# Optimization experiments

Measured on AMD Instinct MI355X. Metric: run time of the kernel, lower is better.

Reference implementation:

```python
import jax, jax.numpy as jnp
import numpy as np

K_SIZE = 5


def extract_patches(x, k):
    """tf.image.extract_patches(SAME, stride 1) -> [B, H, W, k*k, C].

    Kernel offsets are ordered row-major (ki, kj), matching TF's depth
    ordering (ki, kj, c) after the reshape in the original module.
    """
    pad = k // 2
    B, H, W, C = x.shape
    xp = jnp.pad(x, ((0, 0), (pad, pad), (pad, pad), (0, 0)))
    slices = [xp[:, i:i + H, j:j + W, :] for i in range(k) for j in range(k)]
    return jnp.stack(slices, axis=3)  # [B, H, W, k*k, C]


def setup_inputs() -> dict:
    key = jax.random.key(0)
    k1, k2, k3, k4, k5 = jax.random.split(key, 5)
    B, H, C, BIN = 4, 128, 128, 64
    return {
        "main": jax.random.normal(k1, (B, H, H, C), dtype=jnp.float32),
        "ref": jax.random.normal(k2, (B, H, H, C), dtype=jnp.float32),
        "ref_value": jax.random.normal(k3, (B, H, H, BIN), dtype=jnp.float32),
        "W_main": jax.random.normal(k4, (C, C), dtype=jnp.float32) * (2.0 / C) ** 0.5,
        "W_ref": jax.random.normal(k5, (C, C), dtype=jnp.float32) * (2.0 / C) ** 0.5,
    }


def reference(main, ref, ref_value, W_main, W_ref):
    k = K_SIZE
    # 1x1 convolutions (no bias) == per-pixel matmul
    conv_main = jnp.einsum('bhwc,cd->bhwd', main, W_main)
    conv_ref = jnp.einsum('bhwc,cd->bhwd', ref, W_ref)
    # local k x k neighborhood of keys: [B, H, W, k*k, C]
    ref_stacked = extract_patches(conv_ref, k)
    # dot-product attention over the local window
    attn = jnp.einsum('bhwc,bhwkc->bhwk', conv_main, ref_stacked)
    attn = jax.nn.softmax(attn, axis=-1)
    # local k x k neighborhood of values: [B, H, W, k*k, bin]
    ref_value_stacked = extract_patches(ref_value, k)
    # weighted sum of values
    return jnp.einsum('bhwk,bhwki->bhwi', attn, ref_value_stacked)
```

## Files before the change

kernel.cpp:

```cpp
#include <hip/hip_runtime.h>

#define BATCH 4
#define HH 128
#define WW 128
#define CC 128
#define BIN 64
#define NPIX (BATCH * HH * WW)

typedef short bf16x8 __attribute__((ext_vector_type(8)));
typedef float f32x4 __attribute__((ext_vector_type(4)));

__device__ __forceinline__ unsigned bf_hi(float f) {
    unsigned u = __float_as_uint(f);
    return (u + 0x7fffu + ((u >> 16) & 1u)) >> 16;
}
__device__ __forceinline__ uint2 split_aa(float f) {
    unsigned hb = bf_hi(f);
    float lo = f - __uint_as_float(hb << 16);
    unsigned lb = bf_hi(lo);
    return make_uint2(hb | (hb << 16), lb | (lb << 16));
}
__device__ __forceinline__ unsigned split_b(float f) {
    unsigned hb = bf_hi(f);
    float lo = f - __uint_as_float(hb << 16);
    unsigned lb = bf_hi(lo);
    return hb | (lb << 16);
}

#define AROW 72

__global__ __launch_bounds__(256, 4)
void conv_mfma_kernel(const float* __restrict__ Xm, const float* __restrict__ Xr,
                      const float* __restrict__ Wm, const float* __restrict__ Wr,
                      float* __restrict__ Ym, float* __restrict__ Yr) {
    const float* __restrict__ X = blockIdx.y ? Xr : Xm;
    const float* __restrict__ W = blockIdx.y ? Wr : Wm;
    float* __restrict__ Y       = blockIdx.y ? Yr : Ym;

    __shared__ unsigned short AT[128 * AROW];
    __shared__ unsigned short BT[128 * AROW];

    const int t  = threadIdx.x;
    const int wv = t >> 6;
    const int l  = t & 63;
    const int wm = (wv >> 1) * 64;
    const int wn = (wv & 1) * 64;
    const int lr = l & 15;
    const int lq = l >> 4;
    const int p_base = blockIdx.x * 128;

    const int px = t >> 1, ahalf = t & 1;
    const int d  = t & 127, bq = t >> 7;

    f32x4 acc[4][4] = {};

    const float* xbase = X + (size_t)(p_base + px) * CC + ahalf * 8;

    float4 xa0 = *(const float4*)(xbase);
    float4 xa1 = *(const float4*)(xbase + 4);
    float wb0, wb1, wb2, wb3, wb4, wb5, wb6, wb7;
    {
        const float* wp0 = W + (size_t)(bq * 2 * 4) * CC + d;
        wb0 = wp0[0]; wb1 = wp0[CC]; wb2 = wp0[2 * CC]; wb3 = wp0[3 * CC];
        const float* wp1 = W + (size_t)((bq * 2 + 1) * 4) * CC + d;
        wb4 = wp1[0]; wb5 = wp1[CC]; wb6 = wp1[2 * CC]; wb7 = wp1[3 * CC];
    }

    for (int kc = 0; kc < CC; kc += 16) {
        __syncthreads();
        {
            unsigned short* arow = &AT[px * AROW + ahalf * 32];
            {
                uint2 a0 = split_aa(xa0.x), a1 = split_aa(xa0.y),
                      a2 = split_aa(xa0.z), a3 = split_aa(xa0.w);
                *(uint4*)(arow)     = make_uint4(a0.x, a0.y, a1.x, a1.y);
                *(uint4*)(arow + 8) = make_uint4(a2.x, a2.y, a3.x, a3.y);
            }
            {
                uint2 a0 = split_aa(xa1.x), a1 = split_aa(xa1.y),
                      a2 = split_aa(xa1.z), a3 = split_aa(xa1.w);
                *(uint4*)(arow + 16) = make_uint4(a0.x, a0.y, a1.x, a1.y);
                *(uint4*)(arow + 24) = make_uint4(a2.x, a2.y, a3.x, a3.y);
            }
        }
        {
            unsigned b0 = split_b(wb0), b1 = split_b(wb1),
                     b2 = split_b(wb2), b3 = split_b(wb3);
            unsigned short* brow = &BT[d * AROW + (bq * 2) * 16];
            *(uint4*)(brow)     = make_uint4(b0, b0, b1, b1);
            *(uint4*)(brow + 8) = make_uint4(b2, b2, b3, b3);
            unsigned c0 = split_b(wb4), c1 = split_b(wb5),
                     c2 = split_b(wb6), c3 = split_b(wb7);
            unsigned short* brow2 = &BT[d * AROW + (bq * 2 + 1) * 16];
            *(uint4*)(brow2)     = make_uint4(c0, c0, c1, c1);
            *(uint4*)(brow2 + 8) = make_uint4(c2, c2, c3, c3);
        }
        __syncthreads();
        if (kc + 16 < CC) {
            const float* xp = xbase + kc + 16;
            xa0 = *(const float4*)(xp);
            xa1 = *(const float4*)(xp + 4);
            const float* wp0 = W + (size_t)(kc + 16 + bq * 2 * 4) * CC + d;
            wb0 = wp0[0]; wb1 = wp0[CC]; wb2 = wp0[2 * CC]; wb3 = wp0[3 * CC];
            const float* wp1 = W + (size_t)(kc + 16 + (bq * 2 + 1) * 4) * CC + d;
            wb4 = wp1[0]; wb5 = wp1[CC]; wb6 = wp1[2 * CC]; wb7 = wp1[3 * CC];
        }
#pragma unroll
        for (int ks = 0; ks < 2; ++ks) {
            bf16x8 af[4], bfr[4];
#pragma unroll
            for (int mi = 0; mi < 4; ++mi)
                af[mi] = *(const bf16x8*)&AT[(wm + mi * 16 + lr) * AROW + ks * 32 + lq * 8];
#pragma unroll
            for (int ni = 0; ni < 4; ++ni)
                bfr[ni] = *(const bf16x8*)&BT[(wn + ni * 16 + lr) * AROW + ks * 32 + lq * 8];
#pragma unroll
            for (int mi = 0; mi < 4; ++mi)
#pragma unroll
                for (int ni = 0; ni < 4; ++ni)
                    acc[mi][ni] = __builtin_amdgcn_mfma_f32_16x16x32_bf16(
                        af[mi], bfr[ni], acc[mi][ni], 0, 0, 0);
        }
    }

#pragma unroll
    for (int mi = 0; mi < 4; ++mi)
#pragma unroll
        for (int ni = 0; ni < 4; ++ni)
#pragma unroll
            for (int reg = 0; reg < 4; ++reg) {
                const int row = p_base + wm + mi * 16 + lq * 4 + reg;
                Y[(size_t)row * CC + wn + ni * 16 + lr] = acc[mi][ni][reg];
            }
}

#define TH 8
#define TW 16
#define HROW 21
#define GSLOT 257
#define NSLOT (8 * GSLOT)

__global__ __launch_bounds__(256, 1)
void attn_tile_kernel(const float* __restrict__ qm, const float* __restrict__ kr,
                      const float* __restrict__ vv, float* __restrict__ out) {
    __shared__ float4 KS[2][NSLOT];

    const int t    = threadIdx.x;
    const int wid  = t >> 6;
    const int ln   = t & 63;
    const int part = t & 3;
    const int pxi  = t >> 2;

    const int bi = blockIdx.x >> 7;
    const int ty = (blockIdx.x >> 3) & 15;
    const int tx = blockIdx.x & 7;
    const int h0 = ty * TH, w0 = tx * TW;
    const int r  = pxi >> 3;
    const int c2 = (pxi & 7) * 2;
    const int h = h0 + r, w = w0 + c2;
    const int gbase = bi * HH * WW;
    const int pix0 = gbase + h * WW + w;
    const int pix1 = pix0 + 1;
    const int g0 = part * 2;

    unsigned vm0 = 0, vm1 = 0;
#pragma unroll
    for (int dy = 0; dy < 5; ++dy)
#pragma unroll
        for (int dx = 0; dx < 5; ++dx) {
            const int hh = h + dy - 2;
            const int ww0 = w + dx - 2, ww1 = w + 1 + dx - 2;
            if ((unsigned)hh < (unsigned)HH && (unsigned)ww0 < (unsigned)WW)
                vm0 |= 1u << (dy * 5 + dx);
            if ((unsigned)hh < (unsigned)HH && (unsigned)ww1 < (unsigned)WW)
                vm1 |= 1u << (dy * 5 + dx);
        }

    auto stage = [&](int p, int buf) {
        const float* src = (p < 4) ? kr : vv;
        const int ld = (p < 4) ? CC : BIN;
        const int chbase = (p < 4) ? p * 32 : (p - 4) * 32;
#pragma unroll
        for (int j = 0; j < 2; ++j) {
            const int g = wid * 2 + j;
            const int ch = chbase + g * 4;
#pragma unroll
            for (int i = 0; i < 4; ++i) {
                const int slot = i * 64 + ln;
                const int py  = slot / 21;
                const int pxx = slot - py * 21;
                int hh = h0 + py - 2;  hh = hh < 0 ? 0 : (hh > HH - 1 ? HH - 1 : hh);
                int ww = w0 + pxx - 2; ww = ww < 0 ? 0 : (ww > WW - 1 ? WW - 1 : ww);
                const float* gp = src + (size_t)(gbase + hh * WW + ww) * ld + ch;
                __builtin_amdgcn_global_load_lds(
                    (const __attribute__((address_space(1))) void*)gp,
                    (__attribute__((address_space(3))) void*)&KS[buf][g * GSLOT + i * 64],
                    16, 0, 0);
            }
        }
    };

    float lg0[25], lg1[25];
#pragma unroll
    for (int i = 0; i < 25; ++i) { lg0[i] = 0.0f; lg1[i] = 0.0f; }

    stage(0, 0);
    __syncthreads();

    for (int p = 0; p < 6; ++p) {
        if (p < 5) stage(p + 1, (p + 1) & 1);
        const float4* B = KS[p & 1];
        if (p < 4) {
            const float4* qp0 = (const float4*)(qm + (size_t)pix0 * CC + p * 32 + part * 8);
            const float4* qp1 = (const float4*)(qm + (size_t)pix1 * CC + p * 32 + part * 8);
            float4 q00 = qp0[0], q01 = qp0[1];
            float4 q10 = qp1[0], q11 = qp1[1];
#pragma unroll
            for (int dy = 0; dy < 5; ++dy)
#pragma unroll
                for (int du = 0; du < 6; ++du) {
                    const int hp = (r + dy) * HROW + (c2 + du);
                    float4 k0 = B[g0 * GSLOT + hp];
                    float4 k1 = B[g0 * GSLOT + GSLOT + hp];
                    if (du < 5) {
                        lg0[dy * 5 + du] += q00.x * k0.x + q00.y * k0.y +
                                            q00.z * k0.z + q00.w * k0.w +
                                            q01.x * k1.x + q01.y * k1.y +
                                            q01.z * k1.z + q01.w * k1.w;
                    }
                    if (du > 0) {
                        lg1[dy * 5 + du - 1] += q10.x * k0.x + q10.y * k0.y +
                                                q10.z * k0.z + q10.w * k0.w +
                                                q11.x * k1.x + q11.y * k1.y +
                                                q11.z * k1.z + q11.w * k1.w;
                    }
                }
        } else {
            if (p == 4) {
#pragma unroll
                for (int kk = 0; kk < 25; ++kk) {
                    float v0 = lg0[kk];
                    v0 += __shfl_xor(v0, 1);
                    v0 += __shfl_xor(v0, 2);
                    lg0[kk] = v0;
                    float v1 = lg1[kk];
                    v1 += __shfl_xor(v1, 1);
                    v1 += __shfl_xor(v1, 2);
                    lg1[kk] = v1;
                }
#pragma unroll
                for (int kk = 0; kk < 25; ++kk) {
                    if (!((vm0 >> kk) & 1)) lg0[kk] = 0.0f;
                    if (!((vm1 >> kk) & 1)) lg1[kk] = 0.0f;
                }
                float mx0 = lg0[0], mx1 = lg1[0];
#pragma unroll
                for (int kk = 1; kk < 25; ++kk) {
                    mx0 = fmaxf(mx0, lg0[kk]);
                    mx1 = fmaxf(mx1, lg1[kk]);
                }
                float sum0 = 0.0f, sum1 = 0.0f;
#pragma unroll
                for (int kk = 0; kk < 25; ++kk) {
                    lg0[kk] = __expf(lg0[kk] - mx0); sum0 += lg0[kk];
                    lg1[kk] = __expf(lg1[kk] - mx1); sum1 += lg1[kk];
                }
                const float inv0 = 1.0f / sum0, inv1 = 1.0f / sum1;
#pragma unroll
                for (int kk = 0; kk < 25; ++kk) {
                    lg0[kk] = ((vm0 >> kk) & 1) ? lg0[kk] * inv0 : 0.0f;
                    lg1[kk] = ((vm1 >> kk) & 1) ? lg1[kk] * inv1 : 0.0f;
                }
            }
            float4 a00 = make_float4(0.f, 0.f, 0.f, 0.f);
            float4 a01 = make_float4(0.f, 0.f, 0.f, 0.f);
            float4 a10 = make_float4(0.f, 0.f, 0.f, 0.f);
            float4 a11 = make_float4(0.f, 0.f, 0.f, 0.f);
#pragma unroll
            for (int dy = 0; dy < 5; ++dy)
#pragma unroll
                for (int du = 0; du < 6; ++du) {
                    const int hp = (r + dy) * HROW + (c2 + du);
                    float4 v0 = B[g0 * GSLOT + hp];
                    float4 v1 = B[g0 * GSLOT + GSLOT + hp];
                    if (du < 5) {
                        const float wg = lg0[dy * 5 + du];
                        a00.x += wg * v0.x; a00.y += wg * v0.y;
                        a00.z += wg * v0.z; a00.w += wg * v0.w;
                        a01.x += wg * v1.x; a01.y += wg * v1.y;
                        a01.z += wg * v1.z; a01.w += wg * v1.w;
                    }
                    if (du > 0) {
                        const float wg = lg1[dy * 5 + du - 1];
                        a10.x += wg * v0.x; a10.y += wg * v0.y;
                        a10.z += wg * v0.z; a10.w += wg * v0.w;
                        a11.x += wg * v1.x; a11.y += wg * v1.y;
                        a11.z += wg * v1.z; a11.w += wg * v1.w;
                    }
                }
            float4* op0 = (float4*)(out + (size_t)pix0 * BIN + (p - 4) * 32 + part * 8);
            op0[0] = a00;
            op0[1] = a01;
            float4* op1 = (float4*)(out + (size_t)pix1 * BIN + (p - 4) * 32 + part * 8);
            op1[0] = a10;
            op1[1] = a11;
        }
        __syncthreads();
    }
}

extern "C" void kernel_launch(void* const* d_in, const int* in_sizes, int n_in,
                              void* d_out, int out_size, void* d_ws, size_t ws_size,
                              hipStream_t stream) {
    const float* main_in   = (const float*)d_in[0];
    const float* ref_in    = (const float*)d_in[1];
    const float* ref_value = (const float*)d_in[2];
    const float* W_main    = (const float*)d_in[3];
    const float* W_ref     = (const float*)d_in[4];
    float* out = (float*)d_out;

    float* conv_main = (float*)d_ws;
    float* conv_ref  = conv_main + (size_t)NPIX * CC;

    dim3 gconv(NPIX / 128, 2);
    conv_mfma_kernel<<<gconv, 256, 0, stream>>>(main_in, ref_in, W_main, W_ref,
                                                conv_main, conv_ref);

    attn_tile_kernel<<<512, 256, 0, stream>>>(conv_main, conv_ref, ref_value, out);
}
```

Before: 174.0 us.

## Pre-split weights into LDS image and double attention threads per tile

Adds a small pre-kernel that splits both weight matrices into a bf16 hi/lo LDS-layout image, stored temporarily in the output buffer. The conv kernel then copies each weight chunk straight into LDS with global_load_lds instead of converting it per block. The attention kernel moves to 512 threads per block, so each pixel pair is handled by 8 lanes covering 4 channels each, with an extra shuffle step in the reduction and precomputed staging addresses. This cuts redundant weight conversion and raises parallelism, at the cost of an extra launch and higher LDS and register pressure per block.

```diff
diff --git a/kernel.cpp b/kernel.cpp
--- a/kernel.cpp
+++ b/kernel.cpp
@@ -27,15 +27,37 @@
     return hb | (lb << 16);
 }
 
+__global__ __launch_bounds__(256)
+void wsplit_kernel(const float* __restrict__ Wm, const float* __restrict__ Wr,
+                   unsigned short* __restrict__ img) {
+    const int row = blockIdx.x * 256 + threadIdx.x;
+    const int m = row >> 10;
+    const int rr = row & 1023;
+    const int chunk = rr >> 7, d = rr & 127;
+    const float* W = m ? Wr : Wm;
+    unsigned short* rp = img + ((size_t)(m * 8 + chunk) * 128 + d) * 72;
+#pragma unroll
+    for (int cg = 0; cg < 4; ++cg) {
+        const int c = chunk * 16 + cg * 4;
+        unsigned b0 = split_b(W[(size_t)(c + 0) * CC + d]);
+        unsigned b1 = split_b(W[(size_t)(c + 1) * CC + d]);
+        unsigned b2 = split_b(W[(size_t)(c + 2) * CC + d]);
+        unsigned b3 = split_b(W[(size_t)(c + 3) * CC + d]);
+        *(uint4*)(rp + cg * 16)     = make_uint4(b0, b0, b1, b1);
+        *(uint4*)(rp + cg * 16 + 8) = make_uint4(b2, b2, b3, b3);
+    }
+    *(uint4*)(rp + 64) = make_uint4(0, 0, 0, 0);
+}
+
 #define AROW 72
 
 __global__ __launch_bounds__(256, 4)
 void conv_mfma_kernel(const float* __restrict__ Xm, const float* __restrict__ Xr,
-                      const float* __restrict__ Wm, const float* __restrict__ Wr,
+                      const unsigned short* __restrict__ Wimg,
                       float* __restrict__ Ym, float* __restrict__ Yr) {
-    const float* __restrict__ X = blockIdx.y ? Xr : Xm;
-    const float* __restrict__ W = blockIdx.y ? Wr : Wm;
-    float* __restrict__ Y       = blockIdx.y ? Yr : Ym;
+    const int mat = blockIdx.y;
+    const float* __restrict__ X = mat ? Xr : Xm;
+    float* __restrict__ Y       = mat ? Yr : Ym;
 
     __shared__ unsigned short AT[128 * AROW];
     __shared__ unsigned short BT[128 * AROW];
@@ -50,7 +72,6 @@
     const int p_base = blockIdx.x * 128;
 
     const int px = t >> 1, ahalf = t & 1;
-    const int d  = t & 127, bq = t >> 7;
 
     f32x4 acc[4][4] = {};
 
@@ -58,16 +79,18 @@
 
     float4 xa0 = *(const float4*)(xbase);
     float4 xa1 = *(const float4*)(xbase + 4);
-    float wb0, wb1, wb2, wb3, wb4, wb5, wb6, wb7;
-    {
-        const float* wp0 = W + (size_t)(bq * 2 * 4) * CC + d;
-        wb0 = wp0[0]; wb1 = wp0[CC]; wb2 = wp0[2 * CC]; wb3 = wp0[3 * CC];
-        const float* wp1 = W + (size_t)((bq * 2 + 1) * 4) * CC + d;
-        wb4 = wp1[0]; wb5 = wp1[CC]; wb6 = wp1[2 * CC]; wb7 = wp1[3 * CC];
-    }
-
-    for (int kc = 0; kc < CC; kc += 16) {
+
+    for (int kc16 = 0; kc16 < 8; ++kc16) {
         __syncthreads();
+        {
+            const unsigned short* imgrow = Wimg + (size_t)(mat * 8 + kc16) * 9216;
+            for (int i = wv; i < 18; i += 4) {
+                __builtin_amdgcn_global_load_lds(
+                    (const __attribute__((address_space(1))) void*)(imgrow + i * 512 + l * 8),
+                    (__attribute__((address_space(3))) void*)&BT[i * 512],
+                    16, 0, 0);
+            }
+        }
         {
             unsigned short* arow = &AT[px * AROW + ahalf * 32];
             {
@@ -83,27 +106,11 @@
                 *(uint4*)(arow + 24) = make_uint4(a2.x, a2.y, a3.x, a3.y);
             }
         }
-        {
-            unsigned b0 = split_b(wb0), b1 = split_b(wb1),
-                     b2 = split_b(wb2), b3 = split_b(wb3);
-            unsigned short* brow = &BT[d * AROW + (bq * 2) * 16];
-            *(uint4*)(brow)     = make_uint4(b0, b0, b1, b1);
-            *(uint4*)(brow + 8) = make_uint4(b2, b2, b3, b3);
-            unsigned c0 = split_b(wb4), c1 = split_b(wb5),
-                     c2 = split_b(wb6), c3 = split_b(wb7);
-            unsigned short* brow2 = &BT[d * AROW + (bq * 2 + 1) * 16];
-            *(uint4*)(brow2)     = make_uint4(c0, c0, c1, c1);
-            *(uint4*)(brow2 + 8) = make_uint4(c2, c2, c3, c3);
-        }
         __syncthreads();
-        if (kc + 16 < CC) {
-            const float* xp = xbase + kc + 16;
+        if (kc16 < 7) {
+            const float* xp = xbase + kc16 * 16 + 16;
             xa0 = *(const float4*)(xp);
             xa1 = *(const float4*)(xp + 4);
-            const float* wp0 = W + (size_t)(kc + 16 + bq * 2 * 4) * CC + d;
-            wb0 = wp0[0]; wb1 = wp0[CC]; wb2 = wp0[2 * CC]; wb3 = wp0[3 * CC];
-            const float* wp1 = W + (size_t)(kc + 16 + (bq * 2 + 1) * 4) * CC + d;
-            wb4 = wp1[0]; wb5 = wp1[CC]; wb6 = wp1[2 * CC]; wb7 = wp1[3 * CC];
         }
 #pragma unroll
         for (int ks = 0; ks < 2; ++ks) {
@@ -140,7 +147,7 @@
 #define GSLOT 257
 #define NSLOT (8 * GSLOT)
 
-__global__ __launch_bounds__(256, 1)
+__global__ __launch_bounds__(512, 4)
 void attn_tile_kernel(const float* __restrict__ qm, const float* __restrict__ kr,
                       const float* __restrict__ vv, float* __restrict__ out) {
     __shared__ float4 KS[2][NSLOT];
@@ -148,8 +155,8 @@
     const int t    = threadIdx.x;
     const int wid  = t >> 6;
     const int ln   = t & 63;
-    const int part = t & 3;
-    const int pxi  = t >> 2;
+    const int part = t & 7;
+    const int pxi  = t >> 3;
 
     const int bi = blockIdx.x >> 7;
     const int ty = (blockIdx.x >> 3) & 15;
@@ -161,7 +168,6 @@
     const int gbase = bi * HH * WW;
     const int pix0 = gbase + h * WW + w;
     const int pix1 = pix0 + 1;
-    const int g0 = part * 2;
 
     unsigned vm0 = 0, vm1 = 0;
 #pragma unroll
@@ -176,28 +182,37 @@
                 vm1 |= 1u << (dy * 5 + dx);
         }
 
+    int spx0, spx1, spx2, spx3;
+    {
+#pragma unroll
+        for (int i = 0; i < 4; ++i) {
+            const int slot = i * 64 + ln;
+            const int py  = slot / 21;
+            const int pxx = slot - py * 21;
+            int hh = h0 + py - 2;  hh = hh < 0 ? 0 : (hh > HH - 1 ? HH - 1 : hh);
+            int ww = w0 + pxx - 2; ww = ww < 0 ? 0 : (ww > WW - 1 ? WW - 1 : ww);
+            const int pv = gbase + hh * WW + ww;
+            if (i == 0) spx0 = pv; else if (i == 1) spx1 = pv;
+            else if (i == 2) spx2 = pv; else spx3 = pv;
+        }
+    }
+
     auto stage = [&](int p, int buf) {
         const float* src = (p < 4) ? kr : vv;
         const int ld = (p < 4) ? CC : BIN;
-        const int chbase = (p < 4) ? p * 32 : (p - 4) * 32;
-#pragma unroll
-        for (int j = 0; j < 2; ++j) {
-            const int g = wid * 2 + j;
-            const int ch = chbase + g * 4;
-#pragma unroll
-            for (int i = 0; i < 4; ++i) {
-                const int slot = i * 64 + ln;
-                const int py  = slot / 21;
-                const int pxx = slot - py * 21;
-                int hh = h0 + py - 2;  hh = hh < 0 ? 0 : (hh > HH - 1 ? HH - 1 : hh);
-                int ww = w0 + pxx - 2; ww = ww < 0 ? 0 : (ww > WW - 1 ? WW - 1 : ww);
-                const float* gp = src + (size_t)(gbase + hh * WW + ww) * ld + ch;
-                __builtin_amdgcn_global_load_lds(
-                    (const __attribute__((address_space(1))) void*)gp,
-                    (__attribute__((address_space(3))) void*)&KS[buf][g * GSLOT + i * 64],
-                    16, 0, 0);
-            }
-        }
+        const int ch = ((p < 4) ? p * 32 : (p - 4) * 32) + wid * 4;
+        __builtin_amdgcn_global_load_lds(
+            (const __attribute__((address_space(1))) void*)(src + (size_t)spx0 * ld + ch),
+            (__attribute__((address_space(3))) void*)&KS[buf][wid * GSLOT], 16, 0, 0);
+        __builtin_amdgcn_global_load_lds(
+            (const __attribute__((address_space(1))) void*)(src + (size_t)spx1 * ld + ch),
+            (__attribute__((address_space(3))) void*)&KS[buf][wid * GSLOT + 64], 16, 0, 0);
+        __builtin_amdgcn_global_load_lds(
+            (const __attribute__((address_space(1))) void*)(src + (size_t)spx2 * ld + ch),
+            (__attribute__((address_space(3))) void*)&KS[buf][wid * GSLOT + 128], 16, 0, 0);
+        __builtin_amdgcn_global_load_lds(
+            (const __attribute__((address_space(1))) void*)(src + (size_t)spx3 * ld + ch),
+            (__attribute__((address_space(3))) void*)&KS[buf][wid * GSLOT + 192], 16, 0, 0);
     };
 
     float lg0[25], lg1[25];
@@ -209,31 +224,22 @@
 
     for (int p = 0; p < 6; ++p) {
         if (p < 5) stage(p + 1, (p + 1) & 1);
-        const float4* B = KS[p & 1];
+        const float4* Bp = KS[p & 1] + part * GSLOT;
         if (p < 4) {
-            const float4* qp0 = (const float4*)(qm + (size_t)pix0 * CC + p * 32 + part * 8);
-            const float4* qp1 = (const float4*)(qm + (size_t)pix1 * CC + p * 32 + part * 8);
-            float4 q00 = qp0[0], q01 = qp0[1];
-            float4 q10 = qp1[0], q11 = qp1[1];
+            const float4 q0 = *(const float4*)(qm + (size_t)pix0 * CC + p * 32 + part * 4);
+            const float4 q1 = *(const float4*)(qm + (size_t)pix1 * CC + p * 32 + part * 4);
 #pragma unroll
             for (int dy = 0; dy < 5; ++dy)
 #pragma unroll
                 for (int du = 0; du < 6; ++du) {
                     const int hp = (r + dy) * HROW + (c2 + du);
-                    float4 k0 = B[g0 * GSLOT + hp];
-                    float4 k1 = B[g0 * GSLOT + GSLOT + hp];
-                    if (du < 5) {
-                        lg0[dy * 5 + du] += q00.x * k0.x + q00.y * k0.y +
-                                            q00.z * k0.z + q00.w * k0.w +
-                                            q01.x * k1.x + q01.y * k1.y +
-                                            q01.z * k1.z + q01.w * k1.w;
-                    }
-                    if (du > 0) {
-                        lg1[dy * 5 + du - 1] += q10.x * k0.x + q10.y * k0.y +
-                                                q10.z * k0.z + q10.w * k0.w +
-                                                q11.x * k1.x + q11.y * k1.y +
-                                                q11.z * k1.z + q11.w * k1.w;
-                    }
+                    const float4 k = Bp[hp];
+                    if (du < 5)
+                        lg0[dy * 5 + du] += q0.x * k.x + q0.y * k.y +
+                                            q0.z * k.z + q0.w * k.w;
+                    if (du > 0)
+                        lg1[dy * 5 + du - 1] += q1.x * k.x + q1.y * k.y +
+                                                q1.z * k.z + q1.w * k.w;
                 }
         } else {
             if (p == 4) {
@@ -242,10 +248,12 @@
                     float v0 = lg0[kk];
                     v0 += __shfl_xor(v0, 1);
                     v0 += __shfl_xor(v0, 2);
+                    v0 += __shfl_xor(v0, 4);
                     lg0[kk] = v0;
                     float v1 = lg1[kk];
                     v1 += __shfl_xor(v1, 1);
                     v1 += __shfl_xor(v1, 2);
+                    v1 += __shfl_xor(v1, 4);
                     lg1[kk] = v1;
                 }
 #pragma unroll
@@ -272,38 +280,27 @@
                     lg1[kk] = ((vm1 >> kk) & 1) ? lg1[kk] * inv1 : 0.0f;
                 }
             }
-            float4 a00 = make_float4(0.f, 0.f, 0.f, 0.f);
-            float4 a01 = make_float4(0.f, 0.f, 0.f, 0.f);
-            float4 a10 = make_float4(0.f, 0.f, 0.f, 0.f);
-            float4 a11 = make_float4(0.f, 0.f, 0.f, 0.f);
+            float4 a0 = make_float4(0.f, 0.f, 0.f, 0.f);
+            float4 a1 = make_float4(0.f, 0.f, 0.f, 0.f);
 #pragma unroll
             for (int dy = 0; dy < 5; ++dy)
 #pragma unroll
                 for (int du = 0; du < 6; ++du) {
                     const int hp = (r + dy) * HROW + (c2 + du);
-                    float4 v0 = B[g0 * GSLOT + hp];
-                    float4 v1 = B[g0 * GSLOT + GSLOT + hp];
+                    const float4 v = Bp[hp];
                     if (du < 5) {
                         const float wg = lg0[dy * 5 + du];
-                        a00.x += wg * v0.x; a00.y += wg * v0.y;
-                        a00.z += wg * v0.z; a00.w += wg * v0.w;
-                        a01.x += wg * v1.x; a01.y += wg * v1.y;
-                        a01.z += wg * v1.z; a01.w += wg * v1.w;
+                        a0.x += wg * v.x; a0.y += wg * v.y;
+                        a0.z += wg * v.z; a0.w += wg * v.w;
                     }
                     if (du > 0) {
                         const float wg = lg1[dy * 5 + du - 1];
-                        a10.x += wg * v0.x; a10.y += wg * v0.y;
-                        a10.z += wg * v0.z; a10.w += wg * v0.w;
-                        a11.x += wg * v1.x; a11.y += wg * v1.y;
-                        a11.z += wg * v1.z; a11.w += wg * v1.w;
+                        a1.x += wg * v.x; a1.y += wg * v.y;
+                        a1.z += wg * v.z; a1.w += wg * v.w;
                     }
                 }
-            float4* op0 = (float4*)(out + (size_t)pix0 * BIN + (p - 4) * 32 + part * 8);
-            op0[0] = a00;
-            op0[1] = a01;
-            float4* op1 = (float4*)(out + (size_t)pix1 * BIN + (p - 4) * 32 + part * 8);
-            op1[0] = a10;
-            op1[1] = a11;
+            *(float4*)(out + (size_t)pix0 * BIN + (p - 4) * 32 + part * 4) = a0;
+            *(float4*)(out + (size_t)pix1 * BIN + (p - 4) * 32 + part * 4) = a1;
         }
         __syncthreads();
     }
@@ -322,9 +319,12 @@
     float* conv_main = (float*)d_ws;
     float* conv_ref  = conv_main + (size_t)NPIX * CC;
 
+    unsigned short* Wimg = (unsigned short*)d_out;
+    wsplit_kernel<<<8, 256, 0, stream>>>(W_main, W_ref, Wimg);
+
     dim3 gconv(NPIX / 128, 2);
-    conv_mfma_kernel<<<gconv, 256, 0, stream>>>(main_in, ref_in, W_main, W_ref,
+    conv_mfma_kernel<<<gconv, 256, 0, stream>>>(main_in, ref_in, Wimg,
                                                 conv_main, conv_ref);
 
-    attn_tile_kernel<<<512, 256, 0, stream>>>(conv_main, conv_ref, ref_value, out);
-}
+    attn_tile_kernel<<<512, 512, 0, stream>>>(conv_main, conv_ref, ref_value, out);
+}
```

Measured after the change: 224.6 us. 1.29x slower.
